# Optimization experiments

Hardware: AMD Instinct MI355X
Metric: run time of the kernel (lower is better)

The kernel has to match this reference:

```python
import jax, jax.numpy as jnp
import numpy as np

EPS = 1e-7  # K.epsilon()


def setup_inputs() -> dict:
    key = jax.random.key(0)
    B, S, F = 8, 512, 128
    # scale 0.05 keeps un-stabilized exp(x . x_i) finite (diag score ~ ||x||^2)
    x = jax.random.normal(key, (B, S, F), dtype=jnp.float32) * 0.05
    return {"x": x}


def reference(x):
    # Faithful single-shot version of the per-step python loop:
    # for each query step i, scores over all steps s: eij[b,s,i] = x[b,s].x[b,i]
    B, S, F = x.shape
    scores = jnp.einsum('bsf,bif->bsi', x, x)          # (B, S, S)
    e = jnp.exp(scores)                                 # no max-subtraction, as in original
    a = e / (jnp.sum(e, axis=1, keepdims=True) + EPS)   # normalize over s (axis=1)
    ctx = jnp.einsum('bsi,bsf->bif', a, x)              # (B, S, F) attended vector per step i
    # buggy K.tile(temp, [1,1,features_dim]) -> repeats each F-vector F times
    tiled = jnp.tile(ctx, (1, 1, F))                    # (B, S, F*F)
    return jnp.concatenate([x, tiled], axis=-1)         # (B, S, F + F*F)
```

## Files before the change

kernel.cpp:

```cpp
#include <hip/hip_runtime.h>

#define EPS_F 1e-7f

typedef float f4v __attribute__((ext_vector_type(4)));

constexpr int Bb = 8;
constexpr int Ss = 512;
constexpr int Ff = 128;
constexpr int TQ = 8;
constexpr int OUTROW = Ff + Ff * Ff;
constexpr int OUTROW4 = OUTROW / 4;

__global__ __launch_bounds__(256) void attn_fused(const float* __restrict__ x,
                                                  float* __restrict__ out) {
  const int t = threadIdx.x;
  const int bi = blockIdx.x;
  const int b = bi >> 6;
  const int i0 = (bi & 63) * TQ;

  __shared__ float qt[TQ * Ff];
  __shared__ float e[TQ][Ss];
  __shared__ f4v ctx4[TQ][Ff / 4];
  __shared__ float inv_d[TQ];
  __shared__ float red[TQ][4];

  const float* xb = x + (size_t)b * Ss * Ff;

  {
    const f4v* src = (const f4v*)(xb + (size_t)i0 * Ff);
    ((f4v*)qt)[t] = src[t];
  }
  __syncthreads();

  float lsum[TQ];
#pragma unroll
  for (int q = 0; q < TQ; ++q) lsum[q] = 0.f;

  const f4v* q4 = (const f4v*)qt;
  for (int ss = 0; ss < 2; ++ss) {
    const int s = t + ss * 256;
    const f4v* row = (const f4v*)(xb + (size_t)s * Ff);
    float acc[TQ];
#pragma unroll
    for (int q = 0; q < TQ; ++q) acc[q] = 0.f;
#pragma unroll 4
    for (int k = 0; k < Ff / 4; ++k) {
      const f4v v = row[k];
#pragma unroll
      for (int q = 0; q < TQ; ++q) {
        const f4v qv = q4[q * (Ff / 4) + k];
        acc[q] = fmaf(v.x, qv.x, acc[q]);
        acc[q] = fmaf(v.y, qv.y, acc[q]);
        acc[q] = fmaf(v.z, qv.z, acc[q]);
        acc[q] = fmaf(v.w, qv.w, acc[q]);
      }
    }
#pragma unroll
    for (int q = 0; q < TQ; ++q) {
      const float ex = expf(acc[q]);
      e[q][s] = ex;
      lsum[q] += ex;
    }
  }

#pragma unroll
  for (int q = 0; q < TQ; ++q) {
    float v = lsum[q];
#pragma unroll
    for (int off = 32; off > 0; off >>= 1) v += __shfl_down(v, off, 64);
    lsum[q] = v;
  }
  const int lane = t & 63, wid = t >> 6;
  if (lane == 0) {
#pragma unroll
    for (int q = 0; q < TQ; ++q) red[q][wid] = lsum[q];
  }
  __syncthreads();
  if (t < TQ) {
    const float d = ((red[t][0] + red[t][1]) + red[t][2]) + red[t][3];
    inv_d[t] = 1.0f / (d + EPS_F);
  }
  __syncthreads();

  {
    const int f4 = t & 31;
    const int q = t >> 5;
    const f4v* xcol = (const f4v*)xb;
    const float* eq = e[q];
    f4v a = {0.f, 0.f, 0.f, 0.f};
#pragma unroll 4
    for (int s = 0; s < Ss; ++s) {
      const f4v v = xcol[s * 32 + f4];
      const float w = eq[s];
      a.x = fmaf(w, v.x, a.x);
      a.y = fmaf(w, v.y, a.y);
      a.z = fmaf(w, v.z, a.z);
      a.w = fmaf(w, v.w, a.w);
    }
    const float inv = inv_d[q];
    a.x *= inv; a.y *= inv; a.z *= inv; a.w *= inv;
    ctx4[q][f4] = a;
  }
  __syncthreads();

  f4v* out4 = (f4v*)out;
#pragma unroll
  for (int qq = 0; qq < TQ; ++qq) {
    const size_t rb4 = (size_t)(b * Ss + i0 + qq) * OUTROW4;
    if (t < 32) {
      __builtin_nontemporal_store(((const f4v*)qt)[qq * 32 + t],
                                  &out4[rb4 + t]);
    }
    const f4v cv = ctx4[qq][t & 31];
    f4v* dst = out4 + rb4 + 32;
#pragma unroll
    for (int k = 0; k < 16; ++k) {
      __builtin_nontemporal_store(cv, &dst[t + k * 256]);
    }
  }
}

extern "C" void kernel_launch(void* const* d_in, const int* in_sizes, int n_in,
                              void* d_out, int out_size, void* d_ws, size_t ws_size,
                              hipStream_t stream) {
  const float* x = (const float*)d_in[0];
  float* out = (float*)d_out;
  attn_fused<<<dim3(Bb * (Ss / TQ)), dim3(256), 0, stream>>>(x, out);
}
```

Before: 328.3 us.

## Assign one query row per block and split context reduction across thread groups

Result: slower. 373.4 us (+13.7%).

```diff
diff --git a/kernel.cpp b/kernel.cpp
--- a/kernel.cpp
+++ b/kernel.cpp
@@ -7,116 +7,95 @@
 constexpr int Bb = 8;
 constexpr int Ss = 512;
 constexpr int Ff = 128;
-constexpr int TQ = 8;
-constexpr int OUTROW = Ff + Ff * Ff;
-constexpr int OUTROW4 = OUTROW / 4;
+constexpr int OUTROW4 = (Ff + Ff * Ff) / 4;
 
 __global__ __launch_bounds__(256) void attn_fused(const float* __restrict__ x,
                                                   float* __restrict__ out) {
   const int t = threadIdx.x;
   const int bi = blockIdx.x;
-  const int b = bi >> 6;
-  const int i0 = (bi & 63) * TQ;
+  const int b = bi >> 9;
+  const int i = bi & 511;
 
-  __shared__ float qt[TQ * Ff];
-  __shared__ float e[TQ][Ss];
-  __shared__ f4v ctx4[TQ][Ff / 4];
-  __shared__ float inv_d[TQ];
-  __shared__ float red[TQ][4];
+  __shared__ float qrow[Ff];
+  __shared__ float e_lds[Ss];
+  __shared__ f4v part[8][Ff / 4];
+  __shared__ f4v ctx4[Ff / 4];
+  __shared__ float red[4];
+  __shared__ float inv_d_s;
 
   const float* xb = x + (size_t)b * Ss * Ff;
 
-  {
-    const f4v* src = (const f4v*)(xb + (size_t)i0 * Ff);
-    ((f4v*)qt)[t] = src[t];
-  }
+  if (t < Ff / 4) ((f4v*)qrow)[t] = ((const f4v*)(xb + (size_t)i * Ff))[t];
   __syncthreads();
 
-  float lsum[TQ];
-#pragma unroll
-  for (int q = 0; q < TQ; ++q) lsum[q] = 0.f;
-
-  const f4v* q4 = (const f4v*)qt;
+  float lsum = 0.f;
+  const f4v* q4 = (const f4v*)qrow;
   for (int ss = 0; ss < 2; ++ss) {
     const int s = t + ss * 256;
     const f4v* row = (const f4v*)(xb + (size_t)s * Ff);
-    float acc[TQ];
-#pragma unroll
-    for (int q = 0; q < TQ; ++q) acc[q] = 0.f;
-#pragma unroll 4
+    float acc = 0.f;
+#pragma unroll 8
     for (int k = 0; k < Ff / 4; ++k) {
       const f4v v = row[k];
-#pragma unroll
-      for (int q = 0; q < TQ; ++q) {
-        const f4v qv = q4[q * (Ff / 4) + k];
-        acc[q] = fmaf(v.x, qv.x, acc[q]);
-        acc[q] = fmaf(v.y, qv.y, acc[q]);
-        acc[q] = fmaf(v.z, qv.z, acc[q]);
-        acc[q] = fmaf(v.w, qv.w, acc[q]);
-      }
+      const f4v qv = q4[k];
+      acc = fmaf(v.x, qv.x, acc);
+      acc = fmaf(v.y, qv.y, acc);
+      acc = fmaf(v.z, qv.z, acc);
+      acc = fmaf(v.w, qv.w, acc);
     }
-#pragma unroll
-    for (int q = 0; q < TQ; ++q) {
-      const float ex = expf(acc[q]);
-      e[q][s] = ex;
-      lsum[q] += ex;
-    }
+    const float ex = expf(acc);
+    e_lds[s] = ex;
+    lsum += ex;
   }
-
-#pragma unroll
-  for (int q = 0; q < TQ; ++q) {
-    float v = lsum[q];
+  {
+    float v = lsum;
 #pragma unroll
     for (int off = 32; off > 0; off >>= 1) v += __shfl_down(v, off, 64);
-    lsum[q] = v;
-  }
-  const int lane = t & 63, wid = t >> 6;
-  if (lane == 0) {
-#pragma unroll
-    for (int q = 0; q < TQ; ++q) red[q][wid] = lsum[q];
+    if ((t & 63) == 0) red[t >> 6] = v;
   }
   __syncthreads();
-  if (t < TQ) {
-    const float d = ((red[t][0] + red[t][1]) + red[t][2]) + red[t][3];
-    inv_d[t] = 1.0f / (d + EPS_F);
+  if (t == 0) inv_d_s = 1.0f / (((red[0] + red[1]) + (red[2] + red[3])) + EPS_F);
+
+  {
+    const int f4 = t & 31, sg = t >> 5;
+    const f4v* xcol = (const f4v*)xb;
+    const int s0 = sg * 64;
+    f4v a = {0.f, 0.f, 0.f, 0.f};
+#pragma unroll 4
+    for (int s = s0; s < s0 + 64; ++s) {
+      const f4v vv = xcol[s * 32 + f4];
+      const float w = e_lds[s];
+      a.x = fmaf(w, vv.x, a.x);
+      a.y = fmaf(w, vv.y, a.y);
+      a.z = fmaf(w, vv.z, a.z);
+      a.w = fmaf(w, vv.w, a.w);
+    }
+    part[sg][f4] = a;
   }
   __syncthreads();
-
-  {
-    const int f4 = t & 31;
-    const int q = t >> 5;
-    const f4v* xcol = (const f4v*)xb;
-    const float* eq = e[q];
-    f4v a = {0.f, 0.f, 0.f, 0.f};
-#pragma unroll 4
-    for (int s = 0; s < Ss; ++s) {
-      const f4v v = xcol[s * 32 + f4];
-      const float w = eq[s];
-      a.x = fmaf(w, v.x, a.x);
-      a.y = fmaf(w, v.y, a.y);
-      a.z = fmaf(w, v.z, a.z);
-      a.w = fmaf(w, v.w, a.w);
+  if (t < 32) {
+    f4v a = part[0][t];
+#pragma unroll
+    for (int g = 1; g < 8; ++g) {
+      const f4v p = part[g][t];
+      a.x += p.x; a.y += p.y; a.z += p.z; a.w += p.w;
     }
-    const float inv = inv_d[q];
+    const float inv = inv_d_s;
     a.x *= inv; a.y *= inv; a.z *= inv; a.w *= inv;
-    ctx4[q][f4] = a;
+    ctx4[t] = a;
   }
   __syncthreads();
 
   f4v* out4 = (f4v*)out;
+  const size_t rb4 = (size_t)(b * Ss + i) * OUTROW4;
+  if (t < 32) {
+    __builtin_nontemporal_store(((const f4v*)qrow)[t], &out4[rb4 + t]);
+  }
+  const f4v cv = ctx4[t & 31];
+  f4v* dst = out4 + rb4 + 32;
 #pragma unroll
-  for (int qq = 0; qq < TQ; ++qq) {
-    const size_t rb4 = (size_t)(b * Ss + i0 + qq) * OUTROW4;
-    if (t < 32) {
-      __builtin_nontemporal_store(((const f4v*)qt)[qq * 32 + t],
-                                  &out4[rb4 + t]);
-    }
-    const f4v cv = ctx4[qq][t & 31];
-    f4v* dst = out4 + rb4 + 32;
-#pragma unroll
-    for (int k = 0; k < 16; ++k) {
-      __builtin_nontemporal_store(cv, &dst[t + k * 256]);
-    }
+  for (int k = 0; k < 16; ++k) {
+    __builtin_nontemporal_store(cv, &dst[t + k * 256]);
   }
 }
 
@@ -125,5 +104,5 @@
                               hipStream_t stream) {
   const float* x = (const float*)d_in[0];
   float* out = (float*)d_out;
-  attn_fused<<<dim3(Bb * (Ss / TQ)), dim3(256), 0, stream>>>(x, out);
+  attn_fused<<<dim3(Bb * Ss), dim3(256), 0, stream>>>(x, out);
 }
```

## Split attention into compute kernel and wide parallel tiled-output write kernel

Applied to the files above, without the earlier changes.

Result: faster. 296.4 us (-9.7%).

```diff
diff --git a/kernel.cpp b/kernel.cpp
--- a/kernel.cpp
+++ b/kernel.cpp
@@ -8,115 +8,136 @@
 constexpr int Ss = 512;
 constexpr int Ff = 128;
 constexpr int TQ = 8;
-constexpr int OUTROW = Ff + Ff * Ff;
-constexpr int OUTROW4 = OUTROW / 4;
+constexpr int OUTROW4 = (Ff + Ff * Ff) / 4;
 
-__global__ __launch_bounds__(256) void attn_fused(const float* __restrict__ x,
-                                                  float* __restrict__ out) {
+static __device__ __forceinline__ f4v vfma(float w, f4v v, f4v a) {
+  a.x = fmaf(w, v.x, a.x);
+  a.y = fmaf(w, v.y, a.y);
+  a.z = fmaf(w, v.z, a.z);
+  a.w = fmaf(w, v.w, a.w);
+  return a;
+}
+
+__global__ __launch_bounds__(256) void attn_ctx(const float* __restrict__ x,
+                                                float* __restrict__ ctx) {
   const int t = threadIdx.x;
-  const int bi = blockIdx.x;
-  const int b = bi >> 6;
-  const int i0 = (bi & 63) * TQ;
+  const int b = blockIdx.x >> 6;
+  const int i0 = (blockIdx.x & 63) * TQ;
 
-  __shared__ float qt[TQ * Ff];
-  __shared__ float e[TQ][Ss];
-  __shared__ f4v ctx4[TQ][Ff / 4];
+  __shared__ f4v qt4[TQ][Ff / 4];
+  __shared__ f4v e_t4[Ss][2];
+  __shared__ f4v part[8][TQ][Ff / 4];
+  __shared__ float red[4][TQ];
   __shared__ float inv_d[TQ];
-  __shared__ float red[TQ][4];
 
   const float* xb = x + (size_t)b * Ss * Ff;
 
-  {
-    const f4v* src = (const f4v*)(xb + (size_t)i0 * Ff);
-    ((f4v*)qt)[t] = src[t];
-  }
+  ((f4v*)qt4)[t] = ((const f4v*)(xb + (size_t)i0 * Ff))[t];
   __syncthreads();
 
-  float lsum[TQ];
+  float acc0[TQ], acc1[TQ];
 #pragma unroll
-  for (int q = 0; q < TQ; ++q) lsum[q] = 0.f;
-
-  const f4v* q4 = (const f4v*)qt;
-  for (int ss = 0; ss < 2; ++ss) {
-    const int s = t + ss * 256;
-    const f4v* row = (const f4v*)(xb + (size_t)s * Ff);
-    float acc[TQ];
-#pragma unroll
-    for (int q = 0; q < TQ; ++q) acc[q] = 0.f;
+  for (int q = 0; q < TQ; ++q) { acc0[q] = 0.f; acc1[q] = 0.f; }
+  {
+    const f4v* r0 = (const f4v*)(xb + (size_t)t * Ff);
+    const f4v* r1 = (const f4v*)(xb + (size_t)(t + 256) * Ff);
 #pragma unroll 4
     for (int k = 0; k < Ff / 4; ++k) {
-      const f4v v = row[k];
+      const f4v v0 = r0[k], v1 = r1[k];
 #pragma unroll
       for (int q = 0; q < TQ; ++q) {
-        const f4v qv = q4[q * (Ff / 4) + k];
-        acc[q] = fmaf(v.x, qv.x, acc[q]);
-        acc[q] = fmaf(v.y, qv.y, acc[q]);
-        acc[q] = fmaf(v.z, qv.z, acc[q]);
-        acc[q] = fmaf(v.w, qv.w, acc[q]);
+        const f4v qv = qt4[q][k];
+        acc0[q] = fmaf(v0.x, qv.x, acc0[q]);
+        acc0[q] = fmaf(v0.y, qv.y, acc0[q]);
+        acc0[q] = fmaf(v0.z, qv.z, acc0[q]);
+        acc0[q] = fmaf(v0.w, qv.w, acc0[q]);
+        acc1[q] = fmaf(v1.x, qv.x, acc1[q]);
+        acc1[q] = fmaf(v1.y, qv.y, acc1[q]);
+        acc1[q] = fmaf(v1.z, qv.z, acc1[q]);
+        acc1[q] = fmaf(v1.w, qv.w, acc1[q]);
       }
     }
-#pragma unroll
-    for (int q = 0; q < TQ; ++q) {
-      const float ex = expf(acc[q]);
-      e[q][s] = ex;
-      lsum[q] += ex;
-    }
   }
-
+  float e0[TQ], e1[TQ], ls[TQ];
 #pragma unroll
   for (int q = 0; q < TQ; ++q) {
-    float v = lsum[q];
+    e0[q] = expf(acc0[q]);
+    e1[q] = expf(acc1[q]);
+    ls[q] = e0[q] + e1[q];
+  }
+  e_t4[t][0] = (f4v){e0[0], e0[1], e0[2], e0[3]};
+  e_t4[t][1] = (f4v){e0[4], e0[5], e0[6], e0[7]};
+  e_t4[t + 256][0] = (f4v){e1[0], e1[1], e1[2], e1[3]};
+  e_t4[t + 256][1] = (f4v){e1[4], e1[5], e1[6], e1[7]};
+#pragma unroll
+  for (int q = 0; q < TQ; ++q) {
+    float v = ls[q];
 #pragma unroll
     for (int off = 32; off > 0; off >>= 1) v += __shfl_down(v, off, 64);
-    lsum[q] = v;
-  }
-  const int lane = t & 63, wid = t >> 6;
-  if (lane == 0) {
-#pragma unroll
-    for (int q = 0; q < TQ; ++q) red[q][wid] = lsum[q];
+    if ((t & 63) == 0) red[t >> 6][q] = v;
   }
   __syncthreads();
   if (t < TQ) {
-    const float d = ((red[t][0] + red[t][1]) + red[t][2]) + red[t][3];
-    inv_d[t] = 1.0f / (d + EPS_F);
+    inv_d[t] =
+        1.0f / (((red[0][t] + red[1][t]) + (red[2][t] + red[3][t])) + EPS_F);
+  }
+
+  {
+    const int f4 = t & 31, sg = t >> 5;
+    const f4v* xc = (const f4v*)xb;
+    f4v a[TQ];
+#pragma unroll
+    for (int q = 0; q < TQ; ++q) a[q] = (f4v){0.f, 0.f, 0.f, 0.f};
+    const int s0 = sg * 64;
+#pragma unroll 2
+    for (int s = s0; s < s0 + 64; ++s) {
+      const f4v v = xc[s * 32 + f4];
+      const f4v wlo = e_t4[s][0];
+      const f4v whi = e_t4[s][1];
+      a[0] = vfma(wlo.x, v, a[0]);
+      a[1] = vfma(wlo.y, v, a[1]);
+      a[2] = vfma(wlo.z, v, a[2]);
+      a[3] = vfma(wlo.w, v, a[3]);
+      a[4] = vfma(whi.x, v, a[4]);
+      a[5] = vfma(whi.y, v, a[5]);
+      a[6] = vfma(whi.z, v, a[6]);
+      a[7] = vfma(whi.w, v, a[7]);
+    }
+#pragma unroll
+    for (int q = 0; q < TQ; ++q) part[sg][q][f4] = a[q];
   }
   __syncthreads();
 
   {
-    const int f4 = t & 31;
-    const int q = t >> 5;
-    const f4v* xcol = (const f4v*)xb;
-    const float* eq = e[q];
-    f4v a = {0.f, 0.f, 0.f, 0.f};
-#pragma unroll 4
-    for (int s = 0; s < Ss; ++s) {
-      const f4v v = xcol[s * 32 + f4];
-      const float w = eq[s];
-      a.x = fmaf(w, v.x, a.x);
-      a.y = fmaf(w, v.y, a.y);
-      a.z = fmaf(w, v.z, a.z);
-      a.w = fmaf(w, v.w, a.w);
+    const int f4 = t & 31, q = t >> 5;
+    f4v c = part[0][q][f4];
+#pragma unroll
+    for (int g = 1; g < 8; ++g) {
+      const f4v p = part[g][q][f4];
+      c.x += p.x; c.y += p.y; c.z += p.z; c.w += p.w;
     }
     const float inv = inv_d[q];
-    a.x *= inv; a.y *= inv; a.z *= inv; a.w *= inv;
-    ctx4[q][f4] = a;
+    c.x *= inv; c.y *= inv; c.z *= inv; c.w *= inv;
+    ((f4v*)ctx)[(size_t)(b * Ss + i0 + q) * (Ff / 4) + f4] = c;
   }
-  __syncthreads();
+}
 
+__global__ __launch_bounds__(256) void attn_write(const float* __restrict__ x,
+                                                  const float* __restrict__ ctx,
+                                                  float* __restrict__ out) {
+  const int t = threadIdx.x;
+  const size_t row = blockIdx.x;
+  const f4v cv = ((const f4v*)ctx)[row * (Ff / 4) + (t & 31)];
   f4v* out4 = (f4v*)out;
+  const size_t rb4 = row * OUTROW4;
+  if (t < 32) {
+    __builtin_nontemporal_store(((const f4v*)x)[row * (Ff / 4) + t],
+                                &out4[rb4 + t]);
+  }
+  f4v* dst = out4 + rb4 + 32;
 #pragma unroll
-  for (int qq = 0; qq < TQ; ++qq) {
-    const size_t rb4 = (size_t)(b * Ss + i0 + qq) * OUTROW4;
-    if (t < 32) {
-      __builtin_nontemporal_store(((const f4v*)qt)[qq * 32 + t],
-                                  &out4[rb4 + t]);
-    }
-    const f4v cv = ctx4[qq][t & 31];
-    f4v* dst = out4 + rb4 + 32;
-#pragma unroll
-    for (int k = 0; k < 16; ++k) {
-      __builtin_nontemporal_store(cv, &dst[t + k * 256]);
-    }
+  for (int k = 0; k < 16; ++k) {
+    __builtin_nontemporal_store(cv, &dst[t + k * 256]);
   }
 }
 
@@ -125,5 +146,7 @@
                               hipStream_t stream) {
   const float* x = (const float*)d_in[0];
   float* out = (float*)d_out;
-  attn_fused<<<dim3(Bb * (Ss / TQ)), dim3(256), 0, stream>>>(x, out);
+  float* ctx = (float*)d_ws;
+  attn_ctx<<<dim3(Bb * (Ss / TQ)), dim3(256), 0, stream>>>(x, ctx);
+  attn_write<<<dim3(Bb * Ss), dim3(256), 0, stream>>>(x, ctx, out);
 }
```
